# Performance work log

Hardware: AMD Instinct MI355X
Metric: run time of the kernel (lower is better)

## Reference

```python
import jax, jax.numpy as jnp
import numpy as np

N = 100000      # nodes
E = 1600000     # edges (before self-loops)
IN = 128        # in_channels
H = 4           # heads
C = 32          # hidden_channels (per head)
HC = H * C      # 128, LayerNorm dim
NEG_SLOPE = 0.2
LN_EPS = 1e-5


def setup_inputs() -> dict:
    key = jax.random.key(0)
    ks = jax.random.split(key, 8)
    x = jax.random.normal(ks[0], (N, IN), dtype=jnp.float32)
    edge_index = jax.random.randint(ks[1], (2, E), 0, N, dtype=jnp.int64)
    edge_weight = jax.random.uniform(ks[2], (E,), dtype=jnp.float32)
    # GATConv parameters
    W = jax.random.normal(ks[3], (IN, HC), dtype=jnp.float32) * (1.0 / np.sqrt(IN))
    att_src = jax.random.normal(ks[4], (H, C), dtype=jnp.float32) * (1.0 / np.sqrt(C))
    att_dst = jax.random.normal(ks[5], (H, C), dtype=jnp.float32) * (1.0 / np.sqrt(C))
    bias = jnp.zeros((HC,), dtype=jnp.float32)
    # LayerNorm parameters
    gamma = jnp.ones((HC,), dtype=jnp.float32)
    beta = jnp.zeros((HC,), dtype=jnp.float32)
    return {"x": x, "edge_index": edge_index, "edge_weight": edge_weight,
            "W": W, "att_src": att_src, "att_dst": att_dst, "bias": bias,
            "gamma": gamma, "beta": beta}


def reference(x, edge_index, edge_weight, W, att_src, att_dst, bias, gamma, beta):
    # --- GATConv (heads=4, concat, add_self_loops=True) ---
    loops = jnp.arange(N, dtype=edge_index.dtype)
    ei = jnp.concatenate([edge_index, jnp.stack([loops, loops])], axis=1)  # [2, E+N]
    src, dst = ei[0], ei[1]

    xw = (x @ W).reshape(N, H, C)                       # [N, H, C]
    a_src = jnp.sum(xw * att_src, axis=-1)              # [N, H]
    a_dst = jnp.sum(xw * att_dst, axis=-1)              # [N, H]

    # per-edge attention logits, softmax grouped by destination node
    e = jax.nn.leaky_relu(a_src[src] + a_dst[dst], NEG_SLOPE)   # [E+N, H]
    m = jax.ops.segment_max(e, dst, num_segments=N)             # [N, H]
    ex = jnp.exp(e - m[dst])
    denom = jax.ops.segment_sum(ex, dst, num_segments=N)        # [N, H]
    alpha = ex / (denom[dst] + 1e-16)                           # [E+N, H]

    # weighted scatter-add of source features to destinations
    msg = alpha[:, :, None] * xw[src]                           # [E+N, H, C]
    out = jax.ops.segment_sum(msg, dst, num_segments=N)         # [N, H, C]
    out = out.reshape(N, HC) + bias                             # concat heads + bias

    # --- LayerNorm ---
    mu = jnp.mean(out, axis=-1, keepdims=True)
    var = jnp.var(out, axis=-1, keepdims=True)
    return gamma * (out - mu) / jnp.sqrt(var + LN_EPS) + beta
```

## Files before the change

### kernel.cpp

```cpp
#include <hip/hip_runtime.h>
#include <math.h>

#define NN 100000
#define EE 1600000
#define ETOT (EE + NN)
#define NBUK 512
#define NPB 196
#define CHUNK 3125
#define CAP 6144

typedef __attribute__((ext_vector_type(8))) short bf16x8;
typedef __attribute__((ext_vector_type(4))) float f32x4;

__device__ __forceinline__ unsigned short f2bf(float f) {
  unsigned int u = __float_as_uint(f);
  u = u + 0x7fffu + ((u >> 16) & 1u);
  return (unsigned short)(u >> 16);
}

__device__ __forceinline__ float lrelu_exp(float e) {
  e = (e > 0.f) ? e : 0.2f * e;
  return __expf(e);
}

__global__ __launch_bounds__(256) void k_gemm(const float* __restrict__ x,
                                              const float* __restrict__ W,
                                              const float* __restrict__ att_src,
                                              const float* __restrict__ att_dst,
                                              unsigned short* __restrict__ xwb,
                                              float* __restrict__ asrc,
                                              float* __restrict__ adst) {
  __shared__ __align__(16) unsigned short lds[17408];
  __shared__ float satt[256];
  int tid = threadIdx.x;
  for (int i = tid; i < 16384; i += 256) {
    int k = i >> 7, n = i & 127;
    lds[n * 136 + k] = f2bf(W[i]);
  }
  if (tid < 128) satt[tid] = att_src[tid];
  else satt[tid] = att_dst[tid - 128];
  __syncthreads();

  int wv = tid >> 6, lane = tid & 63;
  int m = lane & 15, q = lane >> 4;
  int r = blockIdx.x * 64 + wv * 16 + m;
  bool rok = (r < NN);

  bf16x8 af[4];
#pragma unroll
  for (int kt = 0; kt < 4; kt++) {
    float4 v0 = make_float4(0.f, 0.f, 0.f, 0.f), v1 = v0;
    if (rok) {
      v0 = ((const float4*)x)[(size_t)r * 32 + kt * 8 + q * 2];
      v1 = ((const float4*)x)[(size_t)r * 32 + kt * 8 + q * 2 + 1];
    }
    af[kt][0] = (short)f2bf(v0.x); af[kt][1] = (short)f2bf(v0.y);
    af[kt][2] = (short)f2bf(v0.z); af[kt][3] = (short)f2bf(v0.w);
    af[kt][4] = (short)f2bf(v1.x); af[kt][5] = (short)f2bf(v1.y);
    af[kt][6] = (short)f2bf(v1.z); af[kt][7] = (short)f2bf(v1.w);
  }

  f32x4 acc[8];
#pragma unroll
  for (int nt = 0; nt < 8; nt++) acc[nt] = (f32x4){0.f, 0.f, 0.f, 0.f};

#pragma unroll
  for (int nt = 0; nt < 8; nt++) {
#pragma unroll
    for (int kt = 0; kt < 4; kt++) {
      bf16x8 bf = *((const bf16x8*)&lds[(nt * 16 + m) * 136 + kt * 32 + q * 8]);
      acc[nt] = __builtin_amdgcn_mfma_f32_16x16x32_bf16(af[kt], bf, acc[nt], 0, 0, 0);
    }
  }

  __syncthreads();
#pragma unroll
  for (int nt = 0; nt < 8; nt++)
#pragma unroll
    for (int rg = 0; rg < 4; rg++)
      lds[(wv * 16 + q * 4 + rg) * 128 + nt * 16 + m] = f2bf(acc[nt][rg]);
  __syncthreads();

  size_t base = (size_t)blockIdx.x * 16384;
  const size_t lim = (size_t)NN * 256;
  for (int i = tid; i < 1024; i += 256) {
    size_t off = base + (size_t)i * 16;
    if (off < lim) *((uint4*)((char*)xwb + off)) = ((const uint4*)lds)[i];
  }

  int row = tid >> 2, h = tid & 3;
  int node = blockIdx.x * 64 + row;
  if (node < NN) {
    float ss = 0.f, sd = 0.f;
#pragma unroll
    for (int cq = 0; cq < 4; cq++) {
      uint4 u = *((const uint4*)&lds[row * 128 + h * 32 + cq * 8]);
      int cb = h * 32 + cq * 8;
      float f0 = __uint_as_float(u.x << 16), f1 = __uint_as_float(u.x & 0xffff0000u);
      float f2 = __uint_as_float(u.y << 16), f3 = __uint_as_float(u.y & 0xffff0000u);
      float f4 = __uint_as_float(u.z << 16), f5 = __uint_as_float(u.z & 0xffff0000u);
      float f6 = __uint_as_float(u.w << 16), f7 = __uint_as_float(u.w & 0xffff0000u);
      ss += f0 * satt[cb] + f1 * satt[cb + 1] + f2 * satt[cb + 2] + f3 * satt[cb + 3] +
            f4 * satt[cb + 4] + f5 * satt[cb + 5] + f6 * satt[cb + 6] + f7 * satt[cb + 7];
      sd += f0 * satt[128 + cb] + f1 * satt[128 + cb + 1] + f2 * satt[128 + cb + 2] +
            f3 * satt[128 + cb + 3] + f4 * satt[128 + cb + 4] + f5 * satt[128 + cb + 5] +
            f6 * satt[128 + cb + 6] + f7 * satt[128 + cb + 7];
    }
    asrc[(size_t)node * 4 + h] = ss;
    adst[(size_t)node * 4 + h] = sd;
  }
}

__global__ __launch_bounds__(256) void k_p1(const int* __restrict__ ei,
                                            int* __restrict__ H) {
  __shared__ int h[NBUK];
  int j = blockIdx.x, t = threadIdx.x;
  for (int i = t; i < NBUK; i += 256) h[i] = 0;
  __syncthreads();
  int e0 = j * CHUNK;
  for (int e = e0 + t; e < e0 + CHUNK; e += 256) {
    int d = ei[(size_t)EE + e];
    atomicAdd(&h[d / NPB], 1);
  }
  __syncthreads();
  for (int i = t; i < NBUK; i += 256) H[j * NBUK + i] = h[i];
}

__global__ __launch_bounds__(512) void k_s1(const int* __restrict__ H,
                                            int* __restrict__ R, int* __restrict__ T) {
  __shared__ int s[512];
  int b = blockIdx.x, t = threadIdx.x;
  int v = H[t * NBUK + b];
  s[t] = v;
  __syncthreads();
  for (int off = 1; off < 512; off <<= 1) {
    int tmp = (t >= off) ? s[t - off] : 0;
    __syncthreads();
    s[t] += tmp;
    __syncthreads();
  }
  R[b * 512 + t] = s[t] - v;
  if (t == 511) T[b] = s[511];
}

__global__ __launch_bounds__(512) void k_s2(const int* __restrict__ T,
                                            int* __restrict__ BaseTmp,
                                            int* __restrict__ Base) {
  __shared__ int s[512];
  __shared__ int s2[512];
  int t = threadIdx.x;
  int v = T[t];
  int ncnt = NN - t * NPB;
  ncnt = (ncnt < 0) ? 0 : ((ncnt > NPB) ? NPB : ncnt);
  int w = v + ncnt;
  s[t] = v; s2[t] = w;
  __syncthreads();
  for (int off = 1; off < 512; off <<= 1) {
    int ta = (t >= off) ? s[t - off] : 0;
    int tb = (t >= off) ? s2[t - off] : 0;
    __syncthreads();
    s[t] += ta; s2[t] += tb;
    __syncthreads();
  }
  BaseTmp[t] = s[t] - v;
  Base[t] = s2[t] - w;
}

__global__ __launch_bounds__(256) void k_p3(const int* __restrict__ ei,
                                            const int* __restrict__ R,
                                            const int* __restrict__ BaseTmp,
                                            int* __restrict__ tmpb) {
  __shared__ int cur[NBUK];
  int j = blockIdx.x, t = threadIdx.x;
  for (int b = t; b < NBUK; b += 256) cur[b] = BaseTmp[b] + R[b * 512 + j];
  __syncthreads();
  int e0 = j * CHUNK;
  for (int e = e0 + t; e < e0 + CHUNK; e += 256) {
    int s = ei[e];
    int d = ei[(size_t)EE + e];
    int b = d / NPB;
    int li = d - b * NPB;
    int pos = atomicAdd(&cur[b], 1);
    tmpb[pos] = (li << 17) | s;
  }
}

__global__ __launch_bounds__(256) void k_p4(const int* __restrict__ tmpb,
                                            const int* __restrict__ T,
                                            const int* __restrict__ BaseTmp,
                                            const int* __restrict__ Base,
                                            int* __restrict__ es, int* __restrict__ offs) {
  __shared__ int cnt[256];
  __shared__ int cur[NPB];
  __shared__ int stage[CAP];
  int b = blockIdx.x, t = threadIdx.x;
  if (b == 0 && t == 0) offs[NN] = ETOT;
  int n0 = b * NPB;
  int nloc = NN - n0;
  if (nloc <= 0) return;
  if (nloc > NPB) nloc = NPB;
  int total = T[b];
  int bt = BaseTmp[b], bs = Base[b];
  cnt[t] = (t < nloc) ? 1 : 0;
  __syncthreads();
  for (int e = t; e < total; e += 256) {
    int u = tmpb[bt + e];
    atomicAdd(&cnt[u >> 17], 1);
  }
  __syncthreads();
  int v = cnt[t];
  __syncthreads();
  for (int off = 1; off < 256; off <<= 1) {
    int tmp = (t >= off) ? cnt[t - off] : 0;
    __syncthreads();
    cnt[t] += tmp;
    __syncthreads();
  }
  int excl = cnt[t] - v;
  if (t < nloc) {
    offs[n0 + t] = bs + excl;
    cur[t] = excl + 1;
    if (excl < CAP) stage[excl] = n0 + t;
  }
  __syncthreads();
  for (int e = t; e < total; e += 256) {
    int u = tmpb[bt + e];
    int pos = atomicAdd(&cur[u >> 17], 1);
    if (pos < CAP) stage[pos] = u & 0x1FFFF;
  }
  __syncthreads();
  int btot = total + nloc;
  if (btot > CAP) btot = CAP;
  for (int i = t; i < btot; i += 256) es[bs + i] = stage[i];
}

__global__ __launch_bounds__(256) void k_agg(const unsigned short* __restrict__ xwb,
                                             const float* __restrict__ asrc,
                                             const float* __restrict__ adst,
                                             const int* __restrict__ offs,
                                             const int* __restrict__ es,
                                             const float* __restrict__ bias,
                                             const float* __restrict__ gamma,
                                             const float* __restrict__ beta,
                                             float* __restrict__ out) {
  int lane = threadIdx.x & 63;
  int node = blockIdx.x * 4 + (threadIdx.x >> 6);
  int off0 = offs[node];
  int d = offs[node + 1] - off0;
  int h = lane >> 4;
  int he = lane & 3;
  int c = lane * 2;

  float4 ad4 = *((const float4*)(adst + (size_t)node * 4));
  float adh = (h & 2) ? ((h & 1) ? ad4.w : ad4.z) : ((h & 1) ? ad4.y : ad4.x);
  float ade = (he & 2) ? ((he & 1) ? ad4.w : ad4.z) : ((he & 1) ? ad4.y : ad4.x);

  const unsigned* xp = (const unsigned*)xwb + lane;
  const int* ep = es + off0;
  float ax0 = 0.f, ay0 = 0.f, ax1 = 0.f, ay1 = 0.f;
  float wsum = 0.f;

  int j = 0;
  for (; j + 8 <= d; j += 8) {
    int4 sa = *((const int4*)(ep + j));
    int4 sb = *((const int4*)(ep + j + 4));
    int se = ep[j + (lane >> 3)];
    float av = asrc[(size_t)(unsigned)se * 4u + (unsigned)he];
    unsigned u0 = xp[(unsigned)sa.x * 64u];
    unsigned u1 = xp[(unsigned)sa.y * 64u];
    unsigned u2 = xp[(unsigned)sa.z * 64u];
    unsigned u3 = xp[(unsigned)sa.w * 64u];
    unsigned u4 = xp[(unsigned)sb.x * 64u];
    unsigned u5 = xp[(unsigned)sb.y * 64u];
    unsigned u6 = xp[(unsigned)sb.z * 64u];
    unsigned u7 = xp[(unsigned)sb.w * 64u];
    float wl = lrelu_exp(av + ade);
    float w0 = __shfl(wl, 0 * 8 + h);
    float w1 = __shfl(wl, 1 * 8 + h);
    float w2 = __shfl(wl, 2 * 8 + h);
    float w3 = __shfl(wl, 3 * 8 + h);
    float w4 = __shfl(wl, 4 * 8 + h);
    float w5 = __shfl(wl, 5 * 8 + h);
    float w6 = __shfl(wl, 6 * 8 + h);
    float w7 = __shfl(wl, 7 * 8 + h);
    wsum += ((w0 + w1) + (w2 + w3)) + ((w4 + w5) + (w6 + w7));
    ax0 = fmaf(w0, __uint_as_float(u0 << 16), ax0);
    ay0 = fmaf(w0, __uint_as_float(u0 & 0xffff0000u), ay0);
    ax1 = fmaf(w1, __uint_as_float(u1 << 16), ax1);
    ay1 = fmaf(w1, __uint_as_float(u1 & 0xffff0000u), ay1);
    ax0 = fmaf(w2, __uint_as_float(u2 << 16), ax0);
    ay0 = fmaf(w2, __uint_as_float(u2 & 0xffff0000u), ay0);
    ax1 = fmaf(w3, __uint_as_float(u3 << 16), ax1);
    ay1 = fmaf(w3, __uint_as_float(u3 & 0xffff0000u), ay1);
    ax0 = fmaf(w4, __uint_as_float(u4 << 16), ax0);
    ay0 = fmaf(w4, __uint_as_float(u4 & 0xffff0000u), ay0);
    ax1 = fmaf(w5, __uint_as_float(u5 << 16), ax1);
    ay1 = fmaf(w5, __uint_as_float(u5 & 0xffff0000u), ay1);
    ax0 = fmaf(w6, __uint_as_float(u6 << 16), ax0);
    ay0 = fmaf(w6, __uint_as_float(u6 & 0xffff0000u), ay0);
    ax1 = fmaf(w7, __uint_as_float(u7 << 16), ax1);
    ay1 = fmaf(w7, __uint_as_float(u7 & 0xffff0000u), ay1);
  }
  for (; j < d; ++j) {
    int s0 = ep[j];
    float w = lrelu_exp(asrc[(size_t)(unsigned)s0 * 4u + (unsigned)h] + adh);
    wsum += w;
    unsigned u0 = xp[(unsigned)s0 * 64u];
    ax0 = fmaf(w, __uint_as_float(u0 << 16), ax0);
    ay0 = fmaf(w, __uint_as_float(u0 & 0xffff0000u), ay0);
  }
  float accx = ax0 + ax1, accy = ay0 + ay1;
  float rn = 1.f / (wsum + 1e-16f);

  float vx = accx * rn + bias[c];
  float vy = accy * rn + bias[c + 1];
  float sum = vx + vy, sq = vx * vx + vy * vy;
#pragma unroll
  for (int o = 32; o; o >>= 1) {
    sum += __shfl_xor(sum, o);
    sq += __shfl_xor(sq, o);
  }
  float mean = sum * (1.f / 128.f);
  float var = sq * (1.f / 128.f) - mean * mean;
  float rs = rsqrtf(var + 1e-5f);
  float o0 = gamma[c] * (vx - mean) * rs + beta[c];
  float o1 = gamma[c + 1] * (vy - mean) * rs + beta[c + 1];
  float2 ov; ov.x = o0; ov.y = o1;
  *((float2*)(out + (size_t)node * 128 + c)) = ov;
}

extern "C" void kernel_launch(void* const* d_in, const int* in_sizes, int n_in,
                              void* d_out, int out_size, void* d_ws, size_t ws_size,
                              hipStream_t stream) {
  const float* x = (const float*)d_in[0];
  const int* ei = (const int*)d_in[1];
  const float* W = (const float*)d_in[3];
  const float* att_src = (const float*)d_in[4];
  const float* att_dst = (const float*)d_in[5];
  const float* bias = (const float*)d_in[6];
  const float* gamma = (const float*)d_in[7];
  const float* beta = (const float*)d_in[8];
  float* out = (float*)d_out;

  char* p = (char*)d_ws;
  auto alloc = [&](size_t bytes) -> char* {
    char* r = p;
    p += (bytes + 255) & ~(size_t)255;
    return r;
  };
  unsigned short* xwb = (unsigned short*)alloc((size_t)NN * 128 * 2);
  float* asrc = (float*)alloc((size_t)NN * 4 * 4);
  float* adst = (float*)alloc((size_t)NN * 4 * 4);
  int* es = (int*)alloc((size_t)ETOT * 4);
  int* offs = (int*)alloc((size_t)(NN + 1) * 4);
  int* tmpb = (int*)alloc((size_t)EE * 4);
  int* H = (int*)alloc((size_t)512 * NBUK * 4);
  int* R = (int*)alloc((size_t)NBUK * 512 * 4);
  int* T = (int*)alloc((size_t)NBUK * 4);
  int* BaseTmp = (int*)alloc((size_t)(NBUK + 1) * 4);
  int* Base = (int*)alloc((size_t)(NBUK + 1) * 4);

  k_gemm<<<(NN + 63) / 64, 256, 0, stream>>>(x, W, att_src, att_dst, xwb, asrc, adst);
  k_p1<<<512, 256, 0, stream>>>(ei, H);
  k_s1<<<NBUK, 512, 0, stream>>>(H, R, T);
  k_s2<<<1, 512, 0, stream>>>(T, BaseTmp, Base);
  k_p3<<<512, 256, 0, stream>>>(ei, R, BaseTmp, tmpb);
  k_p4<<<NBUK, 256, 0, stream>>>(tmpb, T, BaseTmp, Base, es, offs);
  k_agg<<<NN / 4, 256, 0, stream>>>(xwb, asrc, adst, offs, es, bias, gamma, beta, out);
}
```

Baseline: 270.6 us.

## Replace bucketed two-level CSR sort with global-atomic counting sort fused into GEMM

After: 387.5 us. 43.2% more time.

```diff
diff --git a/kernel.cpp b/kernel.cpp
--- a/kernel.cpp
+++ b/kernel.cpp
@@ -4,10 +4,7 @@
 #define NN 100000
 #define EE 1600000
 #define ETOT (EE + NN)
-#define NBUK 512
-#define NPB 196
-#define CHUNK 3125
-#define CAP 6144
+#define NBLK 391
 
 typedef __attribute__((ext_vector_type(8))) short bf16x8;
 typedef __attribute__((ext_vector_type(4))) float f32x4;
@@ -23,13 +20,20 @@
   return __expf(e);
 }
 
+__global__ __launch_bounds__(256) void k_zero(int* __restrict__ deg) {
+  int i = blockIdx.x * 256 + threadIdx.x;
+  if (i < NN) deg[i] = 0;
+}
+
 __global__ __launch_bounds__(256) void k_gemm(const float* __restrict__ x,
                                               const float* __restrict__ W,
                                               const float* __restrict__ att_src,
                                               const float* __restrict__ att_dst,
+                                              const int* __restrict__ ei,
                                               unsigned short* __restrict__ xwb,
                                               float* __restrict__ asrc,
-                                              float* __restrict__ adst) {
+                                              float* __restrict__ adst,
+                                              int* __restrict__ deg) {
   __shared__ __align__(16) unsigned short lds[17408];
   __shared__ float satt[256];
   int tid = threadIdx.x;
@@ -109,28 +113,39 @@
     asrc[(size_t)node * 4 + h] = ss;
     adst[(size_t)node * 4 + h] = sd;
   }
-}
-
-__global__ __launch_bounds__(256) void k_p1(const int* __restrict__ ei,
-                                            int* __restrict__ H) {
-  __shared__ int h[NBUK];
-  int j = blockIdx.x, t = threadIdx.x;
-  for (int i = t; i < NBUK; i += 256) h[i] = 0;
-  __syncthreads();
-  int e0 = j * CHUNK;
-  for (int e = e0 + t; e < e0 + CHUNK; e += 256) {
+
+  int gs = gridDim.x * 256;
+  for (int e = blockIdx.x * 256 + tid; e < EE; e += gs) {
     int d = ei[(size_t)EE + e];
-    atomicAdd(&h[d / NPB], 1);
-  }
-  __syncthreads();
-  for (int i = t; i < NBUK; i += 256) H[j * NBUK + i] = h[i];
-}
-
-__global__ __launch_bounds__(512) void k_s1(const int* __restrict__ H,
-                                            int* __restrict__ R, int* __restrict__ T) {
+    atomicAdd(&deg[d], 1);
+  }
+}
+
+__global__ __launch_bounds__(256) void k_scanA(const int* __restrict__ deg,
+                                               int* __restrict__ offs,
+                                               int* __restrict__ T2) {
+  __shared__ int s[256];
+  int b = blockIdx.x, t = threadIdx.x;
+  int n = b * 256 + t;
+  int v = (n < NN) ? deg[n] + 1 : 0;
+  s[t] = v;
+  __syncthreads();
+  for (int off = 1; off < 256; off <<= 1) {
+    int tmp = (t >= off) ? s[t - off] : 0;
+    __syncthreads();
+    s[t] += tmp;
+    __syncthreads();
+  }
+  if (n < NN) offs[n] = s[t] - v;
+  if (t == 255) T2[b] = s[255];
+}
+
+__global__ __launch_bounds__(512) void k_s2b(const int* __restrict__ T2,
+                                             int* __restrict__ Base2,
+                                             int* __restrict__ offs) {
   __shared__ int s[512];
-  int b = blockIdx.x, t = threadIdx.x;
-  int v = H[t * NBUK + b];
+  int t = threadIdx.x;
+  int v = (t < NBLK) ? T2[t] : 0;
   s[t] = v;
   __syncthreads();
   for (int off = 1; off < 512; off <<= 1) {
@@ -139,99 +154,34 @@
     s[t] += tmp;
     __syncthreads();
   }
-  R[b * 512 + t] = s[t] - v;
-  if (t == 511) T[b] = s[511];
-}
-
-__global__ __launch_bounds__(512) void k_s2(const int* __restrict__ T,
-                                            int* __restrict__ BaseTmp,
-                                            int* __restrict__ Base) {
-  __shared__ int s[512];
-  __shared__ int s2[512];
-  int t = threadIdx.x;
-  int v = T[t];
-  int ncnt = NN - t * NPB;
-  ncnt = (ncnt < 0) ? 0 : ((ncnt > NPB) ? NPB : ncnt);
-  int w = v + ncnt;
-  s[t] = v; s2[t] = w;
-  __syncthreads();
-  for (int off = 1; off < 512; off <<= 1) {
-    int ta = (t >= off) ? s[t - off] : 0;
-    int tb = (t >= off) ? s2[t - off] : 0;
-    __syncthreads();
-    s[t] += ta; s2[t] += tb;
-    __syncthreads();
-  }
-  BaseTmp[t] = s[t] - v;
-  Base[t] = s2[t] - w;
-}
-
-__global__ __launch_bounds__(256) void k_p3(const int* __restrict__ ei,
-                                            const int* __restrict__ R,
-                                            const int* __restrict__ BaseTmp,
-                                            int* __restrict__ tmpb) {
-  __shared__ int cur[NBUK];
-  int j = blockIdx.x, t = threadIdx.x;
-  for (int b = t; b < NBUK; b += 256) cur[b] = BaseTmp[b] + R[b * 512 + j];
-  __syncthreads();
-  int e0 = j * CHUNK;
-  for (int e = e0 + t; e < e0 + CHUNK; e += 256) {
+  Base2[t] = s[t] - v;
+  if (t == 0) offs[NN] = ETOT;
+}
+
+__global__ __launch_bounds__(256) void k_scanB(const int* __restrict__ Base2,
+                                               int* __restrict__ offs,
+                                               int* __restrict__ es,
+                                               int* __restrict__ cur) {
+  int b = blockIdx.x, t = threadIdx.x;
+  int n = b * 256 + t;
+  if (n < NN) {
+    int o = offs[n] + Base2[b];
+    offs[n] = o;
+    es[o] = n;
+    cur[n] = o + 1;
+  }
+}
+
+__global__ __launch_bounds__(256) void k_place(const int* __restrict__ ei,
+                                               int* __restrict__ cur,
+                                               int* __restrict__ es) {
+  int gs = gridDim.x * 256;
+  for (int e = blockIdx.x * 256 + threadIdx.x; e < EE; e += gs) {
     int s = ei[e];
     int d = ei[(size_t)EE + e];
-    int b = d / NPB;
-    int li = d - b * NPB;
-    int pos = atomicAdd(&cur[b], 1);
-    tmpb[pos] = (li << 17) | s;
-  }
-}
-
-__global__ __launch_bounds__(256) void k_p4(const int* __restrict__ tmpb,
-                                            const int* __restrict__ T,
-                                            const int* __restrict__ BaseTmp,
-                                            const int* __restrict__ Base,
-                                            int* __restrict__ es, int* __restrict__ offs) {
-  __shared__ int cnt[256];
-  __shared__ int cur[NPB];
-  __shared__ int stage[CAP];
-  int b = blockIdx.x, t = threadIdx.x;
-  if (b == 0 && t == 0) offs[NN] = ETOT;
-  int n0 = b * NPB;
-  int nloc = NN - n0;
-  if (nloc <= 0) return;
-  if (nloc > NPB) nloc = NPB;
-  int total = T[b];
-  int bt = BaseTmp[b], bs = Base[b];
-  cnt[t] = (t < nloc) ? 1 : 0;
-  __syncthreads();
-  for (int e = t; e < total; e += 256) {
-    int u = tmpb[bt + e];
-    atomicAdd(&cnt[u >> 17], 1);
-  }
-  __syncthreads();
-  int v = cnt[t];
-  __syncthreads();
-  for (int off = 1; off < 256; off <<= 1) {
-    int tmp = (t >= off) ? cnt[t - off] : 0;
-    __syncthreads();
-    cnt[t] += tmp;
-    __syncthreads();
-  }
-  int excl = cnt[t] - v;
-  if (t < nloc) {
-    offs[n0 + t] = bs + excl;
-    cur[t] = excl + 1;
-    if (excl < CAP) stage[excl] = n0 + t;
-  }
-  __syncthreads();
-  for (int e = t; e < total; e += 256) {
-    int u = tmpb[bt + e];
-    int pos = atomicAdd(&cur[u >> 17], 1);
-    if (pos < CAP) stage[pos] = u & 0x1FFFF;
-  }
-  __syncthreads();
-  int btot = total + nloc;
-  if (btot > CAP) btot = CAP;
-  for (int i = t; i < btot; i += 256) es[bs + i] = stage[i];
+    int pos = atomicAdd(&cur[d], 1);
+    es[pos] = s;
+  }
 }
 
 __global__ __launch_bounds__(256) void k_agg(const unsigned short* __restrict__ xwb,
@@ -351,20 +301,18 @@
   unsigned short* xwb = (unsigned short*)alloc((size_t)NN * 128 * 2);
   float* asrc = (float*)alloc((size_t)NN * 4 * 4);
   float* adst = (float*)alloc((size_t)NN * 4 * 4);
-  int* es = (int*)alloc((size_t)ETOT * 4);
+  int* es = (int*)alloc((size_t)ETOT * 4 + 128);
   int* offs = (int*)alloc((size_t)(NN + 1) * 4);
-  int* tmpb = (int*)alloc((size_t)EE * 4);
-  int* H = (int*)alloc((size_t)512 * NBUK * 4);
-  int* R = (int*)alloc((size_t)NBUK * 512 * 4);
-  int* T = (int*)alloc((size_t)NBUK * 4);
-  int* BaseTmp = (int*)alloc((size_t)(NBUK + 1) * 4);
-  int* Base = (int*)alloc((size_t)(NBUK + 1) * 4);
-
-  k_gemm<<<(NN + 63) / 64, 256, 0, stream>>>(x, W, att_src, att_dst, xwb, asrc, adst);
-  k_p1<<<512, 256, 0, stream>>>(ei, H);
-  k_s1<<<NBUK, 512, 0, stream>>>(H, R, T);
-  k_s2<<<1, 512, 0, stream>>>(T, BaseTmp, Base);
-  k_p3<<<512, 256, 0, stream>>>(ei, R, BaseTmp, tmpb);
-  k_p4<<<NBUK, 256, 0, stream>>>(tmpb, T, BaseTmp, Base, es, offs);
+  int* deg = (int*)alloc((size_t)NN * 4);
+  int* cur = (int*)alloc((size_t)NN * 4);
+  int* T2 = (int*)alloc((size_t)512 * 4);
+  int* Base2 = (int*)alloc((size_t)512 * 4);
+
+  k_zero<<<NBLK, 256, 0, stream>>>(deg);
+  k_gemm<<<(NN + 63) / 64, 256, 0, stream>>>(x, W, att_src, att_dst, ei, xwb, asrc, adst, deg);
+  k_scanA<<<NBLK, 256, 0, stream>>>(deg, offs, T2);
+  k_s2b<<<1, 512, 0, stream>>>(T2, Base2, offs);
+  k_scanB<<<NBLK, 256, 0, stream>>>(Base2, offs, es, cur);
+  k_place<<<1024, 256, 0, stream>>>(ei, cur, es);
   k_agg<<<NN / 4, 256, 0, stream>>>(xwb, asrc, adst, offs, es, bias, gamma, beta, out);
 }
```
